# Optimization experiments

Hardware: AMD Instinct MI355X
Metric: run time of the kernel (lower is better)

## Reference

```python
import jax, jax.numpy as jnp
import numpy as np

RNN = 2048
NZ = 64
IN = 69  # 54 dofs + 15 actions


def gru_cell(x, h, w_ih, w_hh, b_ih, b_hh):
    gi = x @ w_ih.T + b_ih
    gh = h @ w_hh.T + b_hh
    i_r, i_z, i_n = jnp.split(gi, 3, axis=-1)
    h_r, h_z, h_n = jnp.split(gh, 3, axis=-1)
    r = jax.nn.sigmoid(i_r + h_r)
    z = jax.nn.sigmoid(i_z + h_z)
    n = jnp.tanh(i_n + r * h_n)
    return (1.0 - z) * n + z * h


def setup_inputs() -> dict:
    key = jax.random.key(0)
    ks = jax.random.split(key, 24)
    s = 0.02
    d = {
        'encoder_inputs': jax.random.normal(ks[0], (256, 49, IN), jnp.float32),
        'decoder_inputs': jax.random.normal(ks[1], (256, 25, IN), jnp.float32),
        'eps': jax.random.normal(ks[2], (256, NZ), jnp.float32),
        'fc0_w': jax.random.normal(ks[3], (RNN, 2 * IN), jnp.float32) * s,
        'fc0_b': jnp.zeros((RNN,), jnp.float32),
        'fc1_w': jax.random.normal(ks[4], (RNN, NZ + IN), jnp.float32) * s,
        'fc1_b': jnp.zeros((RNN,), jnp.float32),
        'fc2_w': jax.random.normal(ks[5], (IN, RNN), jnp.float32) * s,
        'fc2_b': jnp.zeros((IN,), jnp.float32),
        'mu_w': jax.random.normal(ks[6], (NZ, RNN), jnp.float32) * s,
        'mu_b': jnp.zeros((NZ,), jnp.float32),
        'sigma_w': jax.random.normal(ks[7], (NZ, RNN), jnp.float32) * s,
        'sigma_b': jnp.zeros((NZ,), jnp.float32),
        'c1_wih': jax.random.normal(ks[8], (3 * RNN, RNN), jnp.float32) * s,
        'c1_whh': jax.random.normal(ks[9], (3 * RNN, RNN), jnp.float32) * s,
        'c1_bih': jnp.zeros((3 * RNN,), jnp.float32),
        'c1_bhh': jnp.zeros((3 * RNN,), jnp.float32),
        'c2_wih': jax.random.normal(ks[10], (3 * RNN, IN), jnp.float32) * s,
        'c2_whh': jax.random.normal(ks[11], (3 * RNN, RNN), jnp.float32) * s,
        'c2_bih': jnp.zeros((3 * RNN,), jnp.float32),
        'c2_bhh': jnp.zeros((3 * RNN,), jnp.float32),
    }
    return d


def reference(encoder_inputs, decoder_inputs, eps, fc0_w, fc0_b, fc1_w, fc1_b, fc2_w, fc2_b,
              mu_w, mu_b, sigma_w, sigma_b, c1_wih, c1_whh, c1_bih, c1_bhh,
              c2_wih, c2_whh, c2_bih, c2_bhh):
    B = encoder_inputs.shape[0]
    enc_t = jnp.transpose(encoder_inputs, (1, 0, 2))  # [S-1, B, IN]
    dec_t = jnp.transpose(decoder_inputs, (1, 0, 2))  # [T, B, IN]
    # encoder step inputs: cat(enc[i], enc[i+1]); last step pairs with dec[0]
    nxt = jnp.concatenate([enc_t[1:], dec_t[:1]], axis=0)
    pairs = jnp.concatenate([enc_t, nxt], axis=-1)  # [S-1, B, 2*IN]
    x = pairs @ fc0_w.T + fc0_b  # fc0, [S-1, B, RNN]
    # precompute input-to-hidden GEMMs for all encoder steps
    gi_all = x @ c1_wih.T + c1_bih  # [S-1, B, 3*RNN]

    def enc_step(h, gi):
        gh = h @ c1_whh.T + c1_bhh
        i_r, i_z, i_n = jnp.split(gi, 3, axis=-1)
        h_r, h_z, h_n = jnp.split(gh, 3, axis=-1)
        r = jax.nn.sigmoid(i_r + h_r)
        z = jax.nn.sigmoid(i_z + h_z)
        n = jnp.tanh(i_n + r * h_n)
        return (1.0 - z) * n + z * h, None

    h0 = jnp.zeros((B, RNN), encoder_inputs.dtype)
    state, _ = jax.lax.scan(enc_step, h0, gi_all)

    z_mu = state @ mu_w.T + mu_b
    z_logvar = state @ sigma_w.T + sigma_b
    z = z_mu + eps * jnp.exp(0.5 * z_logvar)

    dec0 = dec_t[0]  # [B, IN]
    state = jnp.concatenate([z, dec0], axis=-1) @ fc1_w.T + fc1_b

    def dec_step(carry, _):
        h, inp = carry
        h = gru_cell(inp, h, c2_wih, c2_whh, c2_bih, c2_bhh)
        out = inp + (h @ fc2_w.T + fc2_b)  # residual feedback (eval: no dropout)
        return (h, out), out

    T = dec_t.shape[0]
    _, ys = jax.lax.scan(dec_step, (state, dec0), None, length=T)  # [T, B, IN]
    outputs = jnp.transpose(ys, (1, 0, 2))
    return outputs, z_mu, z_logvar
```

## Files before the change

### kernel.cpp

```cpp
#include <hip/hip_runtime.h>
#include <stdint.h>

#define B_    256
#define SE    49
#define TD    25
#define INDIM 69
#define RNN   2048
#define NZ    64
#define G3    6144

typedef __attribute__((ext_vector_type(8))) short short8_t;
typedef __attribute__((ext_vector_type(4))) float f32x4;
typedef unsigned short u16;

#define BARRIER() do { asm volatile("s_waitcnt lgkmcnt(0)" ::: "memory"); \
                       __builtin_amdgcn_s_barrier(); } while (0)

__device__ __forceinline__ u16 f2b(float f) {
  union { float f; unsigned u; } c; c.f = f;
  unsigned u = c.u;
  return (u16)((u + 0x7FFFu + ((u >> 16) & 1u)) >> 16);
}
__device__ __forceinline__ float sigm(float x) { return 1.f / (1.f + __expf(-x)); }
__device__ __forceinline__ short8_t ldbf(const u16* __restrict__ p, size_t off) {
  return *(const short8_t*)&p[off];
}

__device__ __forceinline__ int rmap(int R) {
  int bn = R / 96, rem = R % 96;
  int nw = rem / 48, g = (rem % 48) / 16, jj = rem % 16;
  return g * RNN + bn * 32 + nw * 16 + jj;
}

__global__ void k_reorder(const float* __restrict__ src, u16* __restrict__ dst, int K, int Kp) {
  int total = G3 * Kp;
  for (int i = blockIdx.x * blockDim.x + threadIdx.x; i < total; i += gridDim.x * blockDim.x) {
    int R = i / Kp, c = i % Kp;
    dst[i] = (c < K) ? f2b(src[(size_t)rmap(R) * K + c]) : (u16)0;
  }
}

__global__ void k_fc0T(const float* __restrict__ fc0w, const float* __restrict__ fc0b,
                       u16* __restrict__ dst) {
  int total = 256 * RNN;
  for (int i = blockIdx.x * blockDim.x + threadIdx.x; i < total; i += gridDim.x * blockDim.x) {
    int r = i >> 11, k = i & (RNN - 1);
    float v = 0.f;
    if (r < 2 * INDIM) v = fc0w[(size_t)k * (2 * INDIM) + r];
    else if (r == 2 * INDIM) v = fc0b[k];
    dst[i] = f2b(v);
  }
}

__global__ void k_fc2T(const float* __restrict__ fc2w, u16* __restrict__ dst) {
  int total = 96 * RNN;
  for (int i = blockIdx.x * blockDim.x + threadIdx.x; i < total; i += gridDim.x * blockDim.x) {
    int r = i >> 11, k = i & (RNN - 1);
    dst[i] = (r < INDIM) ? f2b(fc2w[(size_t)r * RNN + k]) : (u16)0;
  }
}

__global__ void k_pairs(const float* __restrict__ enc, const float* __restrict__ dec,
                        u16* __restrict__ pairs) {
  int total = SE * B_ * 256;
  for (int i = blockIdx.x * blockDim.x + threadIdx.x; i < total; i += gridDim.x * blockDim.x) {
    int c = i & 255, rb = i >> 8;
    int b = rb & 255, t = rb >> 8;
    float v = 0.f;
    if (c < INDIM) v = enc[((size_t)b * SE + t) * INDIM + c];
    else if (c < 2 * INDIM) {
      int cc = c - INDIM;
      v = (t < SE - 1) ? enc[((size_t)b * SE + t + 1) * INDIM + cc]
                       : dec[(size_t)b * TD * INDIM + cc];
    } else if (c == 2 * INDIM) v = 1.0f;
    pairs[i] = f2b(v);
  }
}

__global__ void k_msB(const float* __restrict__ muw, const float* __restrict__ sgw,
                      u16* __restrict__ dst) {
  int total = 128 * RNN;
  for (int i = blockIdx.x * blockDim.x + threadIdx.x; i < total; i += gridDim.x * blockDim.x) {
    int n = i >> 11, k = i & (RNN - 1);
    dst[i] = (n < NZ) ? f2b(muw[(size_t)n * RNN + k]) : f2b(sgw[(size_t)(n - NZ) * RNN + k]);
  }
}

__global__ void k_fc1B(const float* __restrict__ w, u16* __restrict__ dst) {
  int total = RNN * 192;
  for (int i = blockIdx.x * blockDim.x + threadIdx.x; i < total; i += gridDim.x * blockDim.x) {
    int n = i / 192, k = i % 192;
    dst[i] = (k < NZ + INDIM) ? f2b(w[(size_t)n * (NZ + INDIM) + k]) : (u16)0;
  }
}

__global__ void k_bias(const float* __restrict__ c1bih, const float* __restrict__ c1bhh,
                       const float* __restrict__ c2wih, const float* __restrict__ fc2b,
                       const float* __restrict__ c2bih, const float* __restrict__ c2bhh,
                       float* __restrict__ ebi, float* __restrict__ ebh,
                       float* __restrict__ dbi0, float* __restrict__ dbi1, float* __restrict__ dbh) {
  int R = blockIdx.x * blockDim.x + threadIdx.x;
  if (R >= G3) return;
  int orig = rmap(R);
  float k3 = 0.f;
  for (int o = 0; o < INDIM; ++o) k3 += c2wih[(size_t)orig * INDIM + o] * fc2b[o];
  ebi[R] = c1bih[orig];
  ebh[R] = c1bhh[orig];
  float d0 = c2bih[orig];
  dbi0[R] = d0;
  dbi1[R] = d0 + k3;
  dbh[R] = c2bhh[orig];
}

__global__ void k_init(float* __restrict__ hf, u16* __restrict__ hbf, float* __restrict__ fbuf,
                       float* __restrict__ omu, float* __restrict__ olv) {
  int i = blockIdx.x * blockDim.x + threadIdx.x;
  if (i < B_ * RNN) { hf[i] = 0.f; hbf[i] = 0; }
  if (i < 3 * B_ * 96) fbuf[i] = 0.f;
  if (i < B_ * NZ) { omu[i] = 0.f; olv[i] = 0.f; }
}

__global__ __launch_bounds__(256) void gemm_bt(
    const u16* __restrict__ A, const u16* __restrict__ W,
    u16* __restrict__ Cb, int N, int K)
{
  constexpr int BM = 128, BN = 128, BK = 64, LDK = BK + 8;
  __shared__ u16 sA[BM * LDK];
  __shared__ u16 sW[BN * LDK];
  const int ntn = N / BN;
  const int bm = blockIdx.x / ntn, bn = blockIdx.x % ntn;
  const int tid = threadIdx.x, lane = tid & 63, wave = tid >> 6;
  const int wr = wave >> 1, wc = wave & 1;
  f32x4 acc[4][4];
#pragma unroll
  for (int i = 0; i < 4; ++i)
#pragma unroll
    for (int j = 0; j < 4; ++j) acc[i][j] = (f32x4)(0.f);
  const int frow = lane & 15, fkq = (lane >> 4) * 8;
  for (int k0 = 0; k0 < K; k0 += BK) {
#pragma unroll
    for (int p = 0; p < 4; ++p) {
      int e = (p * 256 + tid) * 8, r = e / BK, c = e % BK;
      *(short8_t*)&sA[r * LDK + c] = *(const short8_t*)&A[(size_t)(bm * BM + r) * K + k0 + c];
    }
#pragma unroll
    for (int p = 0; p < 4; ++p) {
      int e = (p * 256 + tid) * 8, r = e / BK, c = e % BK;
      *(short8_t*)&sW[r * LDK + c] = *(const short8_t*)&W[(size_t)(bn * BN + r) * K + k0 + c];
    }
    __syncthreads();
#pragma unroll
    for (int kk = 0; kk < BK; kk += 32) {
      short8_t fa[4], fb[4];
#pragma unroll
      for (int m = 0; m < 4; ++m) fa[m] = *(const short8_t*)&sA[(wr * 64 + m * 16 + frow) * LDK + kk + fkq];
#pragma unroll
      for (int n = 0; n < 4; ++n) fb[n] = *(const short8_t*)&sW[(wc * 64 + n * 16 + frow) * LDK + kk + fkq];
#pragma unroll
      for (int m = 0; m < 4; ++m)
#pragma unroll
        for (int n = 0; n < 4; ++n)
          acc[m][n] = __builtin_amdgcn_mfma_f32_16x16x32_bf16(fa[m], fb[n], acc[m][n], 0, 0, 0);
    }
    __syncthreads();
  }
  const int crow = (lane >> 4) * 4, ccol = lane & 15;
#pragma unroll
  for (int n = 0; n < 4; ++n) {
    int col = bn * BN + wc * 64 + n * 16 + ccol;
#pragma unroll
    for (int m = 0; m < 4; ++m)
#pragma unroll
      for (int r = 0; r < 4; ++r) {
        int rowi = bm * BM + wr * 64 + m * 16 + crow + r;
        Cb[(size_t)rowi * N + col] = f2b(acc[m][n][r]);
      }
  }
}

struct Args {
  const u16 *pairs, *Wenc, *whh1, *whh2, *wih2, *fc2T;
  const u16 *msB, *fc1wB;
  const float *ebi, *ebh, *dbi0, *dbi1, *dbh;
  const float *eps, *dec, *fc1_b, *fc2_b, *mu_b, *sg_b;
  float* hf;
  u16*   hbf;
  float* fbuf;
  float* inp;
  u16*   inpbf;
  u16*   fc1xB;
  float *out, *out_mu, *out_lv;
};

__device__ __forceinline__ void compute_gi(const char* sA, const char* sW,
    f32x4 (&aR)[4], f32x4 (&aZ)[4], f32x4 (&aN)[4], int kg, int nw, int lane) {
#pragma unroll
  for (int s = 0; s < 2; ++s) {
    const int L = kg * 8 + s * 4 + (lane >> 4);
    short8_t fa[4], fb[3];
#pragma unroll
    for (int m = 0; m < 4; ++m) {
      int r = m * 16 + (lane & 15);
      fa[m] = *(const short8_t*)&sA[r * 512 + ((L ^ (r & 7)) * 16)];
    }
#pragma unroll
    for (int g = 0; g < 3; ++g) {
      int r = nw * 48 + g * 16 + (lane & 15);
      fb[g] = *(const short8_t*)&sW[r * 512 + ((L ^ (r & 7)) * 16)];
    }
#pragma unroll
    for (int m = 0; m < 4; ++m) {
      aR[m] = __builtin_amdgcn_mfma_f32_16x16x32_bf16(fa[m], fb[0], aR[m], 0, 0, 0);
      aZ[m] = __builtin_amdgcn_mfma_f32_16x16x32_bf16(fa[m], fb[1], aZ[m], 0, 0, 0);
      aN[m] = __builtin_amdgcn_mfma_f32_16x16x32_bf16(fa[m], fb[2], aN[m], 0, 0, 0);
    }
  }
}

__device__ __forceinline__ void compute_gh(const char* base,
    f32x4 (&aR)[4], f32x4 (&aZ)[4], f32x4 (&aN)[4], int kg, int nw, int lane) {
  const char* sA = base;
  const char* sW = base + 16384;
  const int L = kg * 4 + (lane >> 4);
  short8_t fa[4], fb[3];
#pragma unroll
  for (int m = 0; m < 4; ++m) {
    int r = m * 16 + (lane & 15);
    fa[m] = *(const short8_t*)&sA[r * 256 + ((L ^ (r & 15)) * 16)];
  }
#pragma unroll
  for (int g = 0; g < 3; ++g) {
    int r = nw * 48 + g * 16 + (lane & 15);
    fb[g] = *(const short8_t*)&sW[r * 256 + ((L ^ (r & 15)) * 16)];
  }
#pragma unroll
  for (int m = 0; m < 4; ++m) {
    aR[m] = __builtin_amdgcn_mfma_f32_16x16x32_bf16(fa[m], fb[0], aR[m], 0, 0, 0);
    aZ[m] = __builtin_amdgcn_mfma_f32_16x16x32_bf16(fa[m], fb[1], aZ[m], 0, 0, 0);
    aN[m] = __builtin_amdgcn_mfma_f32_16x16x32_bf16(fa[m], fb[2], aN[m], 0, 0, 0);
  }
}

__device__ __forceinline__ void reduce_and_gate(
    f32x4 (&aR)[4], f32x4 (&aZ)[4], f32x4 (&aNI)[4], f32x4 (&aNH)[4],
    char* smem, int tid, int bm, int bn,
    const float* __restrict__ bi, const float* __restrict__ bh,
    const float* __restrict__ hfold, float* __restrict__ hfnew, u16* __restrict__ hbnew) {
  const int lane = tid & 63, wid = tid >> 6;
  auto wr16 = [&](int slots, int w) {
#pragma unroll
    for (int m = 0; m < 4; ++m) {
      *(f32x4*)&smem[(((0 * 4 + m) * slots + w) * 64 + lane) * 16] = aR[m];
      *(f32x4*)&smem[(((1 * 4 + m) * slots + w) * 64 + lane) * 16] = aZ[m];
      *(f32x4*)&smem[(((2 * 4 + m) * slots + w) * 64 + lane) * 16] = aNI[m];
      *(f32x4*)&smem[(((3 * 4 + m) * slots + w) * 64 + lane) * 16] = aNH[m];
    }
  };
  auto add16 = [&](int slots, int w) {
#pragma unroll
    for (int m = 0; m < 4; ++m) {
      aR[m]  += *(const f32x4*)&smem[(((0 * 4 + m) * slots + w) * 64 + lane) * 16];
      aZ[m]  += *(const f32x4*)&smem[(((1 * 4 + m) * slots + w) * 64 + lane) * 16];
      aNI[m] += *(const f32x4*)&smem[(((2 * 4 + m) * slots + w) * 64 + lane) * 16];
      aNH[m] += *(const f32x4*)&smem[(((3 * 4 + m) * slots + w) * 64 + lane) * 16];
    }
  };
  __syncthreads();
  if (wid >= 4) wr16(4, wid - 4);
  __syncthreads();
  if (wid < 4) add16(4, wid);
  __syncthreads();
  if (wid == 2 || wid == 3) wr16(2, wid - 2);
  __syncthreads();
  if (wid < 2) {
    add16(2, wid);
    const int nw = wid, jj = lane & 15;
    const int Rb = bn * 96 + nw * 48;
    const float biR = bi[Rb + jj],      bhR = bh[Rb + jj];
    const float biZ = bi[Rb + 16 + jj], bhZ = bh[Rb + 16 + jj];
    const float biN = bi[Rb + 32 + jj], bhN = bh[Rb + 32 + jj];
    const int j = bn * 32 + nw * 16 + jj;
#pragma unroll
    for (int m = 0; m < 4; ++m)
#pragma unroll
      for (int q = 0; q < 4; ++q) {
        int b = bm * 64 + m * 16 + ((lane >> 4) << 2) + q;
        float r = sigm(aR[m][q] + biR + bhR);
        float z = sigm(aZ[m][q] + biZ + bhZ);
        float nn = 2.f * sigm(2.f * ((aNI[m][q] + biN) + r * (aNH[m][q] + bhN))) - 1.f;
        float hv = (1.f - z) * nn + z * hfold[(size_t)b * RNN + j];
        hfnew[(size_t)b * RNN + j] = hv;
        hbnew[(size_t)b * RNN + j] = f2b(hv);
      }
  }
}

__global__ __launch_bounds__(512, 1) void k_enc(Args a, int t) {
  __shared__ char smem[81920];
  const int tid = threadIdx.x, lane = tid & 63, wid = tid >> 6;
  const int kg = wid >> 1, nw = wid & 1;
  const int bm = blockIdx.x >> 6, bn = blockIdx.x & 63;
  const int rowA0 = bm * 64, rowW0 = bn * 96;
  const int pin = t & 1, pout = pin ^ 1;
  const u16* hin = a.hbf + (size_t)pin * B_ * RNN;
  const float* hfold = a.hf + (size_t)pin * B_ * RNN;
  float* hfnew = a.hf + (size_t)pout * B_ * RNN;
  u16* hbnew = a.hbf + (size_t)pout * B_ * RNN;
  const int sr32 = tid >> 5, sc32 = tid & 31;
  const int sr16 = tid >> 4, sc16 = tid & 15;

  f32x4 aR[4], aZ[4], aNI[4], aNH[4];
#pragma unroll
  for (int m = 0; m < 4; ++m) {
    aR[m] = (f32x4)(0.f); aZ[m] = (f32x4)(0.f);
    aNI[m] = (f32x4)(0.f); aNH[m] = (f32x4)(0.f);
  }

  auto issue_gh = [&](short8_t (&ra)[2], short8_t (&rw)[3], int k0) {
#pragma unroll
    for (int p = 0; p < 2; ++p) {
      int r = p * 32 + sr16;
      ra[p] = ldbf(hin, (size_t)(rowA0 + r) * RNN + k0 + sc16 * 8);
    }
#pragma unroll
    for (int p = 0; p < 3; ++p) {
      int r = p * 32 + sr16;
      rw[p] = ldbf(a.whh1, (size_t)(rowW0 + r) * RNN + k0 + sc16 * 8);
    }
  };
  auto write_gh = [&](char* base, short8_t (&ra)[2], short8_t (&rw)[3]) {
#pragma unroll
    for (int p = 0; p < 2; ++p) {
      int r = p * 32 + sr16;
      *(short8_t*)&base[r * 256 + ((sc16 ^ (r & 15)) * 16)] = ra[p];
    }
#pragma unroll
    for (int p = 0; p < 3; ++p) {
      int r = p * 32 + sr16;
      *(short8_t*)&(base + 16384)[r * 256 + ((sc16 ^ (r & 15)) * 16)] = rw[p];
    }
  };

  {
    const u16* P = a.pairs + (size_t)t * B_ * 256;
    short8_t ga[4], gw[6];
#pragma unroll
    for (int p = 0; p < 4; ++p) {
      int r = p * 16 + sr32;
      ga[p] = ldbf(P, (size_t)(rowA0 + r) * 256 + sc32 * 8);
    }
#pragma unroll
    for (int p = 0; p < 6; ++p) {
      int r = p * 16 + sr32;
      gw[p] = ldbf(a.Wenc, (size_t)(rowW0 + r) * 256 + sc32 * 8);
    }
#pragma unroll
    for (int p = 0; p < 4; ++p) {
      int r = p * 16 + sr32;
      *(short8_t*)&smem[r * 512 + ((sc32 ^ (r & 7)) * 16)] = ga[p];
    }
#pragma unroll
    for (int p = 0; p < 6; ++p) {
      int r = p * 16 + sr32;
      *(short8_t*)&smem[32768 + r * 512 + ((sc32 ^ (r & 7)) * 16)] = gw[p];
    }
  }
  short8_t rA0[2], rW0[3], rA1[2], rW1[3];
  issue_gh(rA0, rW0, 0);
  issue_gh(rA1, rW1, 128);
  BARRIER();
  compute_gi(smem, smem + 32768, aR, aZ, aNI, kg, nw, lane);
  BARRIER();
  write_gh(smem, rA0, rW0);
  issue_gh(rA0, rW0, 2 * 128);
  BARRIER();
#pragma unroll
  for (int i = 0; i < 16; ++i) {
    char* cb = (i & 1) ? smem + 40960 : smem;
    if (i + 1 <= 15) {
      char* nb = ((i + 1) & 1) ? smem + 40960 : smem;
      if ((i + 1) & 1) {
        write_gh(nb, rA1, rW1);
        if (i + 3 <= 15) issue_gh(rA1, rW1, (i + 3) * 128);
      } else {
        write_gh(nb, rA0, rW0);
        if (i + 3 <= 15) issue_gh(rA0, rW0, (i + 3) * 128);
      }
    }
    compute_gh(cb, aR, aZ, aNH, kg, nw, lane);
    if (i < 15) BARRIER();
  }
  reduce_and_gate(aR, aZ, aNI, aNH, smem, tid, bm, bn, a.ebi, a.ebh, hfold, hfnew, hbnew);
}

__global__ __launch_bounds__(512, 1) void k_dec(Args a, int t) {
  __shared__ char smem[81920];
  const int tid = threadIdx.x, lane = tid & 63, wid = tid >> 6;
  const int kg = wid >> 1, nw = wid & 1;
  const int bm = blockIdx.x >> 6, bn = blockIdx.x & 63;
  const int rowA0 = bm * 64, rowW0 = bn * 96;
  const int pin = t & 1, pout = pin ^ 1;
  const int irs = (t + 1) & 1, iws = t & 1;
  const int frd = (t + 2) % 3;
  const u16* hin = a.hbf + (size_t)pin * B_ * RNN;
  const float* hfold = a.hf + (size_t)pin * B_ * RNN;
  float* hfnew = a.hf + (size_t)pout * B_ * RNN;
  u16* hbnew = a.hbf + (size_t)pout * B_ * RNN;
  const int gtid = blockIdx.x * 512 + tid;
  const int sr32 = tid >> 5, sc32 = tid & 31;
  const int sr16 = tid >> 4, sc16 = tid & 15;
  const int fr = lane & 15, fq = (lane >> 4) << 3;

  if (t >= 1 && gtid < B_ * INDIM) {
    int b = gtid / INDIM, o = gtid % INDIM;
    float v = a.inp[(size_t)irs * B_ * INDIM + gtid] +
              a.fbuf[(size_t)frd * B_ * 96 + b * 96 + o] + a.fc2_b[o];
    a.out[((size_t)b * TD + (t - 1)) * INDIM + o] = v;
    a.inp[(size_t)iws * B_ * INDIM + gtid] = v;
    a.inpbf[(size_t)iws * B_ * 128 + b * 128 + o] = f2b(v);
  }
  if (gtid < B_ * 96)
    a.fbuf[(size_t)((t + 1) % 3) * B_ * 96 + gtid] = 0.f;

  f32x4 aR[4], aZ[4], aNI[4], aNH[4];
#pragma unroll
  for (int m = 0; m < 4; ++m) {
    aR[m] = (f32x4)(0.f); aZ[m] = (f32x4)(0.f);
    aNI[m] = (f32x4)(0.f); aNH[m] = (f32x4)(0.f);
  }

  auto issue_gh = [&](short8_t (&ra)[2], short8_t (&rw)[3], int k0) {
#pragma unroll
    for (int p = 0; p < 2; ++p) {
      int r = p * 32 + sr16;
      ra[p] = ldbf(hin, (size_t)(rowA0 + r) * RNN + k0 + sc16 * 8);
    }
#pragma unroll
    for (int p = 0; p < 3; ++p) {
      int r = p * 32 + sr16;
      rw[p] = ldbf(a.whh2, (size_t)(rowW0 + r) * RNN + k0 + sc16 * 8);
    }
  };
  auto write_gh = [&](char* base, short8_t (&ra)[2], short8_t (&rw)[3]) {
#pragma unroll
    for (int p = 0; p < 2; ++p) {
      int r = p * 32 + sr16;
      *(short8_t*)&base[r * 256 + ((sc16 ^ (r & 15)) * 16)] = ra[p];
    }
#pragma unroll
    for (int p = 0; p < 3; ++p) {
      int r = p * 32 + sr16;
      *(short8_t*)&(base + 16384)[r * 256 + ((sc16 ^ (r & 15)) * 16)] = rw[p];
    }
  };

  {
    const u16* inpA = a.inpbf + (size_t)irs * B_ * 128;
    const float* F = a.fbuf + (size_t)frd * B_ * 96;
    short8_t ga[4], gw[6];
#pragma unroll
    for (int p = 0; p < 4; ++p) {
      int r = p * 16 + sr32;
      if (sc32 < 16) {
        ga[p] = ldbf(inpA, (size_t)(rowA0 + r) * 128 + sc32 * 8);
      } else {
        short8_t v;
        int o0 = (sc32 - 16) * 8;
#pragma unroll
        for (int e = 0; e < 8; ++e) {
          int o = o0 + e;
          float fv = (o < 96) ? F[(size_t)(rowA0 + r) * 96 + o] : 0.f;
          v[e] = (short)f2b(fv);
        }
        ga[p] = v;
      }
    }
#pragma unroll
    for (int p = 0; p < 6; ++p) {
      int r = p * 16 + sr32;
      gw[p] = ldbf(a.wih2, (size_t)(rowW0 + r) * 128 + (sc32 & 15) * 8);
    }
#pragma unroll
    for (int p = 0; p < 4; ++p) {
      int r = p * 16 + sr32;
      *(short8_t*)&smem[r * 512 + ((sc32 ^ (r & 7)) * 16)] = ga[p];
    }
#pragma unroll
    for (int p = 0; p < 6; ++p) {
      int r = p * 16 + sr32;
      *(short8_t*)&smem[32768 + r * 512 + ((sc32 ^ (r & 7)) * 16)] = gw[p];
    }
  }
  short8_t rA0[2], rW0[3], rA1[2], rW1[3];
  issue_gh(rA0, rW0, 0);
  issue_gh(rA1, rW1, 128);
  BARRIER();
  compute_gi(smem, smem + 32768, aR, aZ, aNI, kg, nw, lane);
  BARRIER();
  write_gh(smem, rA0, rW0);
  issue_gh(rA0, rW0, 2 * 128);
  BARRIER();
#pragma unroll
  for (int i = 0; i < 16; ++i) {
    char* cb = (i & 1) ? smem + 40960 : smem;
    if (i + 1 <= 15) {
      char* nb = ((i + 1) & 1) ? smem + 40960 : smem;
      if ((i + 1) & 1) {
        write_gh(nb, rA1, rW1);
        if (i + 3 <= 15) issue_gh(rA1, rW1, (i + 3) * 128);
      } else {
        write_gh(nb, rA0, rW0);
        if (i + 3 <= 15) issue_gh(rA0, rW0, (i + 3) * 128);
      }
    }
    compute_gh(cb, aR, aZ, aNH, kg, nw, lane);
    if (i < 15) BARRIER();
  }
  reduce_and_gate(aR, aZ, aNI, aNH, smem, tid, bm, bn,
                  (t >= 1) ? a.dbi1 : a.dbi0, a.dbh, hfold, hfnew, hbnew);

  __syncthreads();
  if (wid < 4) {
    const int wr = wid >> 1, wc = wid & 1;
    const int kcol = bn * 32 + fq;
    short8_t fa[2], fb[3];
#pragma unroll
    for (int m = 0; m < 2; ++m)
      fa[m] = ldbf(hbnew, (size_t)(bm * 64 + wr * 32 + m * 16 + fr) * RNN + kcol);
#pragma unroll
    for (int n = 0; n < 3; ++n)
      fb[n] = ldbf(a.fc2T, (size_t)(wc * 48 + n * 16 + fr) * RNN + kcol);
    f32x4 accf[2][3];
#pragma unroll
    for (int m = 0; m < 2; ++m)
#pragma unroll
      for (int n = 0; n < 3; ++n) accf[m][n] = (f32x4)(0.f);
#pragma unroll
    for (int m = 0; m < 2; ++m)
#pragma unroll
      for (int n = 0; n < 3; ++n)
        accf[m][n] = __builtin_amdgcn_mfma_f32_16x16x32_bf16(fa[m], fb[n], accf[m][n], 0, 0, 0);
    float* fdst = a.fbuf + (size_t)(t % 3) * B_ * 96;
#pragma unroll
    for (int m = 0; m < 2; ++m)
#pragma unroll
      for (int n = 0; n < 3; ++n)
#pragma unroll
        for (int q = 0; q < 4; ++q) {
          int row = bm * 64 + wr * 32 + m * 16 + ((lane >> 4) << 2) + q;
          int col = wc * 48 + n * 16 + (lane & 15);
          atomicAdd(&fdst[row * 96 + col], accf[m][n][q]);
        }
  }
}

__global__ __launch_bounds__(256) void k_msm(Args a) {
  const int bm = blockIdx.x >> 3, kc = blockIdx.x & 7;
  const int lane = threadIdx.x & 63, wid = threadIdx.x >> 6;
  const int wr = wid >> 1, wc = wid & 1;
  const int fr = lane & 15, fq = (lane >> 4) << 3;
  const u16* h1 = a.hbf + (size_t)B_ * RNN;
  f32x4 acc[4][4];
#pragma unroll
  for (int m = 0; m < 4; ++m)
#pragma unroll
    for (int n = 0; n < 4; ++n) acc[m][n] = (f32x4)(0.f);
#pragma unroll
  for (int ks = 0; ks < 8; ++ks) {
    const int k = kc * 256 + ks * 32 + fq;
    short8_t fa[4], fb[4];
#pragma unroll
    for (int m = 0; m < 4; ++m)
      fa[m] = ldbf(h1, (size_t)(bm * 128 + wr * 64 + m * 16 + fr) * RNN + k);
#pragma unroll
    for (int n = 0; n < 4; ++n)
      fb[n] = ldbf(a.msB, (size_t)(wc * 64 + n * 16 + fr) * RNN + k);
#pragma unroll
    for (int m = 0; m < 4; ++m)
#pragma unroll
      for (int n = 0; n < 4; ++n)
        acc[m][n] = __builtin_amdgcn_mfma_f32_16x16x32_bf16(fa[m], fb[n], acc[m][n], 0, 0, 0);
  }
#pragma unroll
  for (int m = 0; m < 4; ++m)
#pragma unroll
    for (int n = 0; n < 4; ++n)
#pragma unroll
      for (int q = 0; q < 4; ++q) {
        int row = bm * 128 + wr * 64 + m * 16 + ((lane >> 4) << 2) + q;
        int col = wc * 64 + n * 16 + (lane & 15);
        if (col < NZ) atomicAdd(&a.out_mu[row * NZ + col], acc[m][n][q]);
        else          atomicAdd(&a.out_lv[row * NZ + col - NZ], acc[m][n][q]);
      }
}

__global__ void k_sample(Args a) {
  int gid = blockIdx.x * blockDim.x + threadIdx.x;
  if (gid < B_ * NZ) {
    int b = gid >> 6, n = gid & 63;
    float mu = a.out_mu[gid] + a.mu_b[n];
    float lv = a.out_lv[gid] + a.sg_b[n];
    a.out_mu[gid] = mu;
    a.out_lv[gid] = lv;
    a.fc1xB[b * 192 + n] = f2b(mu + a.eps[gid] * __expf(0.5f * lv));
  }
  if (gid < B_ * 128) {
    int b = gid >> 7, c = gid & 127;
    float v = (c < INDIM) ? a.dec[(size_t)b * TD * INDIM + c] : 0.f;
    u16 vb = f2b(v);
    a.inpbf[(size_t)b * 128 + c] = vb;
    a.inpbf[(size_t)B_ * 128 + b * 128 + c] = vb;
    if (c < INDIM) {
      a.inp[b * INDIM + c] = v;
      a.inp[B_ * INDIM + b * INDIM + c] = v;
      a.fc1xB[b * 192 + NZ + c] = f2b(v);
    }
  }
  if (gid < B_ * 192) {
    int c = gid % 192;
    if (c >= NZ + INDIM) a.fc1xB[gid] = 0;
  }
}

__global__ __launch_bounds__(256) void k_fc1m(Args a) {
  const int bm = blockIdx.x >> 4, bn = blockIdx.x & 15;
  const int lane = threadIdx.x & 63, wid = threadIdx.x >> 6;
  const int wr = wid >> 1, wc = wid & 1;
  const int fr = lane & 15, fq = (lane >> 4) << 3;
  f32x4 acc[4][4];
#pragma unroll
  for (int m = 0; m < 4; ++m)
#pragma unroll
    for (int n = 0; n < 4; ++n) acc[m][n] = (f32x4)(0.f);
#pragma unroll
  for (int ks = 0; ks < 6; ++ks) {
    const int k = ks * 32 + fq;
    short8_t fa[4], fb[4];
#pragma unroll
    for (int m = 0; m < 4; ++m)
      fa[m] = ldbf(a.fc1xB, (size_t)(bm * 128 + wr * 64 + m * 16 + fr) * 192 + k);
#pragma unroll
    for (int n = 0; n < 4; ++n)
      fb[n] = ldbf(a.fc1wB, (size_t)(bn * 128 + wc * 64 + n * 16 + fr) * 192 + k);
#pragma unroll
    for (int m = 0; m < 4; ++m)
#pragma unroll
      for (int n = 0; n < 4; ++n)
        acc[m][n] = __builtin_amdgcn_mfma_f32_16x16x32_bf16(fa[m], fb[n], acc[m][n], 0, 0, 0);
  }
#pragma unroll
  for (int n = 0; n < 4; ++n) {
    const int col = bn * 128 + wc * 64 + n * 16 + (lane & 15);
    const float bv = a.fc1_b[col];
#pragma unroll
    for (int m = 0; m < 4; ++m)
#pragma unroll
      for (int q = 0; q < 4; ++q) {
        int row = bm * 128 + wr * 64 + m * 16 + ((lane >> 4) << 2) + q;
        float v = acc[m][n][q] + bv;
        a.hf[(size_t)row * RNN + col] = v;
        a.hbf[(size_t)row * RNN + col] = f2b(v);
      }
  }
}

__global__ void k_tail(Args a) {
  int i = blockIdx.x * blockDim.x + threadIdx.x;
  if (i < B_ * INDIM) {
    int b = i / INDIM, o = i % INDIM;
    float v = a.inp[(size_t)(24 & 1) * B_ * INDIM + i] +
              a.fbuf[(size_t)(24 % 3) * B_ * 96 + b * 96 + o] + a.fc2_b[o];
    a.out[((size_t)b * TD + 24) * INDIM + o] = v;
  }
}

extern "C" void kernel_launch(void* const* d_in, const int* in_sizes, int n_in,
                              void* d_out, int out_size, void* d_ws, size_t ws_size,
                              hipStream_t stream)
{
  const float* enc    = (const float*)d_in[0];
  const float* dec    = (const float*)d_in[1];
  const float* eps    = (const float*)d_in[2];
  const float* fc0_w  = (const float*)d_in[3];
  const float* fc0_b  = (const float*)d_in[4];
  const float* fc1_w  = (const float*)d_in[5];
  const float* fc1_b  = (const float*)d_in[6];
  const float* fc2_w  = (const float*)d_in[7];
  const float* fc2_b  = (const float*)d_in[8];
  const float* mu_w   = (const float*)d_in[9];
  const float* mu_b   = (const float*)d_in[10];
  const float* sg_w   = (const float*)d_in[11];
  const float* sg_b   = (const float*)d_in[12];
  const float* c1_wih = (const float*)d_in[13];
  const float* c1_whh = (const float*)d_in[14];
  const float* c1_bih = (const float*)d_in[15];
  const float* c1_bhh = (const float*)d_in[16];
  const float* c2_wih = (const float*)d_in[17];
  const float* c2_whh = (const float*)d_in[18];
  const float* c2_bih = (const float*)d_in[19];
  const float* c2_bhh = (const float*)d_in[20];

  float* out_outputs = (float*)d_out;
  float* out_mu = out_outputs + (size_t)B_ * TD * INDIM;
  float* out_lv = out_mu + (size_t)B_ * NZ;

  char* ws = (char*)d_ws;
  size_t off = 0;
  auto alloc = [&](size_t bytes) -> void* {
    void* p = ws + off; off += (bytes + 255) & ~(size_t)255; return p;
  };

  u16* whh1_r = (u16*)alloc((size_t)G3 * RNN * 2);
  u16* whh2_r = (u16*)alloc((size_t)G3 * RNN * 2);
  u16* wih1_r = (u16*)alloc((size_t)G3 * RNN * 2);
  u16* wih2_r = (u16*)alloc((size_t)G3 * 128 * 2);
  u16* fc0T   = (u16*)alloc((size_t)256 * RNN * 2);
  u16* fc2T   = (u16*)alloc((size_t)96 * RNN * 2);
  u16* Wenc   = (u16*)alloc((size_t)G3 * 256 * 2);
  u16* pairs  = (u16*)alloc((size_t)SE * B_ * 256 * 2);
  u16* msB    = (u16*)alloc((size_t)128 * RNN * 2);
  u16* fc1wB  = (u16*)alloc((size_t)RNN * 192 * 2);
  float* hf   = (float*)alloc((size_t)2 * B_ * RNN * 4);
  u16* hbf    = (u16*)alloc((size_t)2 * B_ * RNN * 2);
  float* fbuf = (float*)alloc((size_t)3 * B_ * 96 * 4);
  float* inp  = (float*)alloc((size_t)2 * B_ * INDIM * 4);
  u16* inpbf  = (u16*)alloc((size_t)2 * B_ * 128 * 2);
  u16* fc1xB  = (u16*)alloc((size_t)B_ * 192 * 2);
  float* ebi  = (float*)alloc((size_t)G3 * 4);
  float* ebh  = (float*)alloc((size_t)G3 * 4);
  float* dbi0 = (float*)alloc((size_t)G3 * 4);
  float* dbi1 = (float*)alloc((size_t)G3 * 4);
  float* dbh  = (float*)alloc((size_t)G3 * 4);
  (void)ws_size; (void)in_sizes; (void)n_in; (void)out_size;

  k_reorder<<<4096, 256, 0, stream>>>(c1_whh, whh1_r, RNN, RNN);
  k_reorder<<<4096, 256, 0, stream>>>(c2_whh, whh2_r, RNN, RNN);
  k_reorder<<<4096, 256, 0, stream>>>(c1_wih, wih1_r, RNN, RNN);
  k_reorder<<<1024, 256, 0, stream>>>(c2_wih, wih2_r, INDIM, 128);
  k_fc0T<<<512, 256, 0, stream>>>(fc0_w, fc0_b, fc0T);
  k_fc2T<<<256, 256, 0, stream>>>(fc2_w, fc2T);
  k_pairs<<<2048, 256, 0, stream>>>(enc, dec, pairs);
  k_msB<<<256, 256, 0, stream>>>(mu_w, sg_w, msB);
  k_fc1B<<<256, 256, 0, stream>>>(fc1_w, fc1wB);
  k_bias<<<24, 256, 0, stream>>>(c1_bih, c1_bhh, c2_wih, fc2_b, c2_bih, c2_bhh,
                                 ebi, ebh, dbi0, dbi1, dbh);

  Args a;
  a.pairs = pairs; a.Wenc = Wenc; a.whh1 = whh1_r; a.whh2 = whh2_r;
  a.wih2 = wih2_r; a.fc2T = fc2T; a.msB = msB; a.fc1wB = fc1wB;
  a.ebi = ebi; a.ebh = ebh; a.dbi0 = dbi0; a.dbi1 = dbi1; a.dbh = dbh;
  a.eps = eps; a.dec = dec; a.fc1_b = fc1_b; a.fc2_b = fc2_b;
  a.mu_b = mu_b; a.sg_b = sg_b;
  a.hf = hf; a.hbf = hbf; a.fbuf = fbuf; a.inp = inp; a.inpbf = inpbf;
  a.fc1xB = fc1xB; a.out = out_outputs; a.out_mu = out_mu; a.out_lv = out_lv;

  k_init<<<2048, 256, 0, stream>>>(hf, hbf, fbuf, out_mu, out_lv);
  gemm_bt<<<(G3 / 128) * (256 / 128), 256, 0, stream>>>(wih1_r, fc0T, Wenc, 256, RNN);

  for (int t = 0; t < SE; ++t)
    k_enc<<<256, 512, 0, stream>>>(a, t);
  k_msm<<<16, 256, 0, stream>>>(a);
  k_sample<<<192, 256, 0, stream>>>(a);
  k_fc1m<<<32, 256, 0, stream>>>(a);
  for (int t = 0; t < TD; ++t)
    k_dec<<<256, 512, 0, stream>>>(a, t);
  k_tail<<<69, 256, 0, stream>>>(a);
}
```

Measured before the change: 1.435 ms.

## Double waves per block in GRU step kernels by splitting batch rows across waves

The encoder and decoder recurrent-step kernels go from 512 to 1024 threads per block. Each wave now computes a 32-row by 48-column tile instead of 64 by 48, and the tile load/store indexing is rebalanced across the larger thread count. The cross-wave K reduction is reorganised for four K-groups times four M/N sub-tiles. The intent is more waves per CU, so the latency of the one-block-per-CU recurrence is better hidden. In exchange each wave has fewer MFMAs per LDS fragment load, the reduction stage carries more traffic, and the main loop is no longer force-unrolled.

```diff
diff --git a/kernel.cpp b/kernel.cpp
--- a/kernel.cpp
+++ b/kernel.cpp
@@ -192,99 +192,52 @@
   float *out, *out_mu, *out_lv;
 };
 
-__device__ __forceinline__ void compute_gi(const char* sA, const char* sW,
-    f32x4 (&aR)[4], f32x4 (&aZ)[4], f32x4 (&aN)[4], int kg, int nw, int lane) {
-#pragma unroll
-  for (int s = 0; s < 2; ++s) {
-    const int L = kg * 8 + s * 4 + (lane >> 4);
-    short8_t fa[4], fb[3];
-#pragma unroll
-    for (int m = 0; m < 4; ++m) {
-      int r = m * 16 + (lane & 15);
-      fa[m] = *(const short8_t*)&sA[r * 512 + ((L ^ (r & 7)) * 16)];
-    }
-#pragma unroll
-    for (int g = 0; g < 3; ++g) {
-      int r = nw * 48 + g * 16 + (lane & 15);
-      fb[g] = *(const short8_t*)&sW[r * 512 + ((L ^ (r & 7)) * 16)];
-    }
-#pragma unroll
-    for (int m = 0; m < 4; ++m) {
-      aR[m] = __builtin_amdgcn_mfma_f32_16x16x32_bf16(fa[m], fb[0], aR[m], 0, 0, 0);
-      aZ[m] = __builtin_amdgcn_mfma_f32_16x16x32_bf16(fa[m], fb[1], aZ[m], 0, 0, 0);
-      aN[m] = __builtin_amdgcn_mfma_f32_16x16x32_bf16(fa[m], fb[2], aN[m], 0, 0, 0);
-    }
-  }
-}
-
-__device__ __forceinline__ void compute_gh(const char* base,
-    f32x4 (&aR)[4], f32x4 (&aZ)[4], f32x4 (&aN)[4], int kg, int nw, int lane) {
-  const char* sA = base;
-  const char* sW = base + 16384;
-  const int L = kg * 4 + (lane >> 4);
-  short8_t fa[4], fb[3];
-#pragma unroll
-  for (int m = 0; m < 4; ++m) {
-    int r = m * 16 + (lane & 15);
-    fa[m] = *(const short8_t*)&sA[r * 256 + ((L ^ (r & 15)) * 16)];
-  }
-#pragma unroll
-  for (int g = 0; g < 3; ++g) {
-    int r = nw * 48 + g * 16 + (lane & 15);
-    fb[g] = *(const short8_t*)&sW[r * 256 + ((L ^ (r & 15)) * 16)];
-  }
-#pragma unroll
-  for (int m = 0; m < 4; ++m) {
-    aR[m] = __builtin_amdgcn_mfma_f32_16x16x32_bf16(fa[m], fb[0], aR[m], 0, 0, 0);
-    aZ[m] = __builtin_amdgcn_mfma_f32_16x16x32_bf16(fa[m], fb[1], aZ[m], 0, 0, 0);
-    aN[m] = __builtin_amdgcn_mfma_f32_16x16x32_bf16(fa[m], fb[2], aN[m], 0, 0, 0);
-  }
-}
-
 __device__ __forceinline__ void reduce_and_gate(
-    f32x4 (&aR)[4], f32x4 (&aZ)[4], f32x4 (&aNI)[4], f32x4 (&aNH)[4],
+    f32x4 (&aR)[2], f32x4 (&aZ)[2], f32x4 (&aNI)[2], f32x4 (&aNH)[2],
     char* smem, int tid, int bm, int bn,
     const float* __restrict__ bi, const float* __restrict__ bh,
     const float* __restrict__ hfold, float* __restrict__ hfnew, u16* __restrict__ hbnew) {
   const int lane = tid & 63, wid = tid >> 6;
-  auto wr16 = [&](int slots, int w) {
-#pragma unroll
-    for (int m = 0; m < 4; ++m) {
-      *(f32x4*)&smem[(((0 * 4 + m) * slots + w) * 64 + lane) * 16] = aR[m];
-      *(f32x4*)&smem[(((1 * 4 + m) * slots + w) * 64 + lane) * 16] = aZ[m];
-      *(f32x4*)&smem[(((2 * 4 + m) * slots + w) * 64 + lane) * 16] = aNI[m];
-      *(f32x4*)&smem[(((3 * 4 + m) * slots + w) * 64 + lane) * 16] = aNH[m];
-    }
-  };
-  auto add16 = [&](int slots, int w) {
-#pragma unroll
-    for (int m = 0; m < 4; ++m) {
-      aR[m]  += *(const f32x4*)&smem[(((0 * 4 + m) * slots + w) * 64 + lane) * 16];
-      aZ[m]  += *(const f32x4*)&smem[(((1 * 4 + m) * slots + w) * 64 + lane) * 16];
-      aNI[m] += *(const f32x4*)&smem[(((2 * 4 + m) * slots + w) * 64 + lane) * 16];
-      aNH[m] += *(const f32x4*)&smem[(((3 * 4 + m) * slots + w) * 64 + lane) * 16];
+  const int kg = wid >> 2, grp = wid & 3;
+  auto wrp = [&](int slots, int s) {
+#pragma unroll
+    for (int m = 0; m < 2; ++m) {
+      *(f32x4*)&smem[(((0 * 2 + m) * slots + s) * 64 + lane) * 16] = aR[m];
+      *(f32x4*)&smem[(((1 * 2 + m) * slots + s) * 64 + lane) * 16] = aZ[m];
+      *(f32x4*)&smem[(((2 * 2 + m) * slots + s) * 64 + lane) * 16] = aNI[m];
+      *(f32x4*)&smem[(((3 * 2 + m) * slots + s) * 64 + lane) * 16] = aNH[m];
+    }
+  };
+  auto addp = [&](int slots, int s) {
+#pragma unroll
+    for (int m = 0; m < 2; ++m) {
+      aR[m]  += *(const f32x4*)&smem[(((0 * 2 + m) * slots + s) * 64 + lane) * 16];
+      aZ[m]  += *(const f32x4*)&smem[(((1 * 2 + m) * slots + s) * 64 + lane) * 16];
+      aNI[m] += *(const f32x4*)&smem[(((2 * 2 + m) * slots + s) * 64 + lane) * 16];
+      aNH[m] += *(const f32x4*)&smem[(((3 * 2 + m) * slots + s) * 64 + lane) * 16];
     }
   };
   __syncthreads();
-  if (wid >= 4) wr16(4, wid - 4);
+  if (kg >= 2) wrp(8, (kg - 2) * 4 + grp);
   __syncthreads();
-  if (wid < 4) add16(4, wid);
+  if (kg < 2) addp(8, kg * 4 + grp);
   __syncthreads();
-  if (wid == 2 || wid == 3) wr16(2, wid - 2);
+  if (kg == 1) wrp(4, grp);
   __syncthreads();
-  if (wid < 2) {
-    add16(2, wid);
-    const int nw = wid, jj = lane & 15;
+  if (kg == 0) {
+    addp(4, grp);
+    const int mw = grp & 1, nw = grp >> 1;
+    const int jj = lane & 15;
     const int Rb = bn * 96 + nw * 48;
     const float biR = bi[Rb + jj],      bhR = bh[Rb + jj];
     const float biZ = bi[Rb + 16 + jj], bhZ = bh[Rb + 16 + jj];
     const float biN = bi[Rb + 32 + jj], bhN = bh[Rb + 32 + jj];
     const int j = bn * 32 + nw * 16 + jj;
 #pragma unroll
-    for (int m = 0; m < 4; ++m)
+    for (int m = 0; m < 2; ++m)
 #pragma unroll
       for (int q = 0; q < 4; ++q) {
-        int b = bm * 64 + m * 16 + ((lane >> 4) << 2) + q;
+        int b = bm * 64 + mw * 32 + m * 16 + ((lane >> 4) << 2) + q;
         float r = sigm(aR[m][q] + biR + bhR);
         float z = sigm(aZ[m][q] + biZ + bhZ);
         float nn = 2.f * sigm(2.f * ((aNI[m][q] + biN) + r * (aNH[m][q] + bhN))) - 1.f;
@@ -295,86 +248,128 @@
   }
 }
 
-__global__ __launch_bounds__(512, 1) void k_enc(Args a, int t) {
+__global__ __launch_bounds__(1024, 1) void k_enc(Args a, int t) {
   __shared__ char smem[81920];
   const int tid = threadIdx.x, lane = tid & 63, wid = tid >> 6;
-  const int kg = wid >> 1, nw = wid & 1;
+  const int mw = wid & 1, nw = (wid >> 1) & 1, kg = wid >> 2;
   const int bm = blockIdx.x >> 6, bn = blockIdx.x & 63;
-  const int rowA0 = bm * 64, rowW0 = bn * 96;
+  const int rowA0 = bm * 64, rowW0b = bn * 96;
   const int pin = t & 1, pout = pin ^ 1;
   const u16* hin = a.hbf + (size_t)pin * B_ * RNN;
   const float* hfold = a.hf + (size_t)pin * B_ * RNN;
   float* hfnew = a.hf + (size_t)pout * B_ * RNN;
   u16* hbnew = a.hbf + (size_t)pout * B_ * RNN;
-  const int sr32 = tid >> 5, sc32 = tid & 31;
-  const int sr16 = tid >> 4, sc16 = tid & 15;
-
-  f32x4 aR[4], aZ[4], aNI[4], aNH[4];
-#pragma unroll
-  for (int m = 0; m < 4; ++m) {
+
+  f32x4 aR[2], aZ[2], aNI[2], aNH[2];
+#pragma unroll
+  for (int m = 0; m < 2; ++m) {
     aR[m] = (f32x4)(0.f); aZ[m] = (f32x4)(0.f);
     aNI[m] = (f32x4)(0.f); aNH[m] = (f32x4)(0.f);
   }
 
-  auto issue_gh = [&](short8_t (&ra)[2], short8_t (&rw)[3], int k0) {
+  auto issue_gh = [&](short8_t& ra, short8_t (&rw)[2], int k0) {
+    { int r = tid >> 4, c = tid & 15;
+      ra = ldbf(hin, (size_t)(rowA0 + r) * RNN + k0 + c * 8); }
 #pragma unroll
     for (int p = 0; p < 2; ++p) {
-      int r = p * 32 + sr16;
-      ra[p] = ldbf(hin, (size_t)(rowA0 + r) * RNN + k0 + sc16 * 8);
-    }
-#pragma unroll
-    for (int p = 0; p < 3; ++p) {
-      int r = p * 32 + sr16;
-      rw[p] = ldbf(a.whh1, (size_t)(rowW0 + r) * RNN + k0 + sc16 * 8);
-    }
-  };
-  auto write_gh = [&](char* base, short8_t (&ra)[2], short8_t (&rw)[3]) {
+      int s = tid + p * 1024;
+      if (s < 1536) {
+        int r = s >> 4, c = s & 15;
+        rw[p] = ldbf(a.whh1, (size_t)(rowW0b + r) * RNN + k0 + c * 8);
+      }
+    }
+  };
+  auto write_gh = [&](char* base, short8_t& ra, short8_t (&rw)[2]) {
+    { int r = tid >> 4, c = tid & 15;
+      *(short8_t*)&base[r * 256 + ((c ^ (r & 15)) * 16)] = ra; }
 #pragma unroll
     for (int p = 0; p < 2; ++p) {
-      int r = p * 32 + sr16;
-      *(short8_t*)&base[r * 256 + ((sc16 ^ (r & 15)) * 16)] = ra[p];
-    }
-#pragma unroll
-    for (int p = 0; p < 3; ++p) {
-      int r = p * 32 + sr16;
-      *(short8_t*)&(base + 16384)[r * 256 + ((sc16 ^ (r & 15)) * 16)] = rw[p];
+      int s = tid + p * 1024;
+      if (s < 1536) {
+        int r = s >> 4, c = s & 15;
+        *(short8_t*)&(base + 16384)[r * 256 + ((c ^ (r & 15)) * 16)] = rw[p];
+      }
+    }
+  };
+  auto compute_gh = [&](const char* base) {
+    const char* sA = base;
+    const char* sW = base + 16384;
+    const int L = kg * 4 + (lane >> 4);
+    short8_t fa[2], fb[3];
+#pragma unroll
+    for (int m = 0; m < 2; ++m) {
+      int r = mw * 32 + m * 16 + (lane & 15);
+      fa[m] = *(const short8_t*)&sA[r * 256 + ((L ^ (r & 15)) * 16)];
+    }
+#pragma unroll
+    for (int g = 0; g < 3; ++g) {
+      int r = nw * 48 + g * 16 + (lane & 15);
+      fb[g] = *(const short8_t*)&sW[r * 256 + ((L ^ (r & 15)) * 16)];
+    }
+#pragma unroll
+    for (int m = 0; m < 2; ++m) {
+      aR[m]  = __builtin_amdgcn_mfma_f32_16x16x32_bf16(fa[m], fb[0], aR[m], 0, 0, 0);
+      aZ[m]  = __builtin_amdgcn_mfma_f32_16x16x32_bf16(fa[m], fb[1], aZ[m], 0, 0, 0);
+      aNH[m] = __builtin_amdgcn_mfma_f32_16x16x32_bf16(fa[m], fb[2], aNH[m], 0, 0, 0);
+    }
+  };
+  auto compute_gi = [&]() {
+#pragma unroll
+    for (int s = 0; s < 2; ++s) {
+      const int L = kg * 8 + s * 4 + (lane >> 4);
+      short8_t fa[2], fb[3];
+#pragma unroll
+      for (int m = 0; m < 2; ++m) {
+        int r = mw * 32 + m * 16 + (lane & 15);
+        fa[m] = *(const short8_t*)&smem[r * 512 + ((L ^ (r & 7)) * 16)];
+      }
+#pragma unroll
+      for (int g = 0; g < 3; ++g) {
+        int r = nw * 48 + g * 16 + (lane & 15);
+        fb[g] = *(const short8_t*)&(smem + 32768)[r * 512 + ((L ^ (r & 7)) * 16)];
+      }
+#pragma unroll
+      for (int m = 0; m < 2; ++m) {
+        aR[m]  = __builtin_amdgcn_mfma_f32_16x16x32_bf16(fa[m], fb[0], aR[m], 0, 0, 0);
+        aZ[m]  = __builtin_amdgcn_mfma_f32_16x16x32_bf16(fa[m], fb[1], aZ[m], 0, 0, 0);
+        aNI[m] = __builtin_amdgcn_mfma_f32_16x16x32_bf16(fa[m], fb[2], aNI[m], 0, 0, 0);
+      }
     }
   };
 
   {
     const u16* P = a.pairs + (size_t)t * B_ * 256;
-    short8_t ga[4], gw[6];
-#pragma unroll
-    for (int p = 0; p < 4; ++p) {
-      int r = p * 16 + sr32;
-      ga[p] = ldbf(P, (size_t)(rowA0 + r) * 256 + sc32 * 8);
-    }
-#pragma unroll
-    for (int p = 0; p < 6; ++p) {
-      int r = p * 16 + sr32;
-      gw[p] = ldbf(a.Wenc, (size_t)(rowW0 + r) * 256 + sc32 * 8);
-    }
-#pragma unroll
-    for (int p = 0; p < 4; ++p) {
-      int r = p * 16 + sr32;
-      *(short8_t*)&smem[r * 512 + ((sc32 ^ (r & 7)) * 16)] = ga[p];
-    }
-#pragma unroll
-    for (int p = 0; p < 6; ++p) {
-      int r = p * 16 + sr32;
-      *(short8_t*)&smem[32768 + r * 512 + ((sc32 ^ (r & 7)) * 16)] = gw[p];
-    }
-  }
-  short8_t rA0[2], rW0[3], rA1[2], rW1[3];
+    short8_t ga[2], gw[3];
+#pragma unroll
+    for (int p = 0; p < 2; ++p) {
+      int s = tid + p * 1024, r = s >> 5, c = s & 31;
+      ga[p] = ldbf(P, (size_t)(rowA0 + r) * 256 + c * 8);
+    }
+#pragma unroll
+    for (int p = 0; p < 3; ++p) {
+      int s = tid + p * 1024, r = s >> 5, c = s & 31;
+      gw[p] = ldbf(a.Wenc, (size_t)(rowW0b + r) * 256 + c * 8);
+    }
+#pragma unroll
+    for (int p = 0; p < 2; ++p) {
+      int s = tid + p * 1024, r = s >> 5, c = s & 31;
+      *(short8_t*)&smem[r * 512 + ((c ^ (r & 7)) * 16)] = ga[p];
+    }
+#pragma unroll
+    for (int p = 0; p < 3; ++p) {
+      int s = tid + p * 1024, r = s >> 5, c = s & 31;
+      *(short8_t*)&(smem + 32768)[r * 512 + ((c ^ (r & 7)) * 16)] = gw[p];
+    }
+  }
+  short8_t rA0, rW0[2], rA1, rW1[2];
   issue_gh(rA0, rW0, 0);
   issue_gh(rA1, rW1, 128);
   BARRIER();
-  compute_gi(smem, smem + 32768, aR, aZ, aNI, kg, nw, lane);
+  compute_gi();
   BARRIER();
   write_gh(smem, rA0, rW0);
-  issue_gh(rA0, rW0, 2 * 128);
+  issue_gh(rA0, rW0, 256);
   BARRIER();
-#pragma unroll
   for (int i = 0; i < 16; ++i) {
     char* cb = (i & 1) ? smem + 40960 : smem;
     if (i + 1 <= 15) {
@@ -387,18 +382,19 @@
         if (i + 3 <= 15) issue_gh(rA0, rW0, (i + 3) * 128);
       }
     }
-    compute_gh(cb, aR, aZ, aNH, kg, nw, lane);
+    compute_gh(cb);
     if (i < 15) BARRIER();
   }
   reduce_and_gate(aR, aZ, aNI, aNH, smem, tid, bm, bn, a.ebi, a.ebh, hfold, hfnew, hbnew);
 }
 
-__global__ __launch_bounds__(512, 1) void k_dec(Args a, int t) {
+__global__ __launch_bounds__(1024, 1) void k_dec(Args a, int t) {
   __shared__ char smem[81920];
   const int tid = threadIdx.x, lane = tid & 63, wid = tid >> 6;
-  const int kg = wid >> 1, nw = wid & 1;
+  const int mw = wid & 1, nw = (wid >> 1) & 1, kg = wid >> 2;
   const int bm = blockIdx.x >> 6, bn = blockIdx.x & 63;
-  const int rowA0 = bm * 64, rowW0 = bn * 96;
+  const int rowA0 = bm * 64, rowW0b = bn * 96;
+  const int fr = lane & 15, fq = (lane >> 4) << 3;
   const int pin = t & 1, pout = pin ^ 1;
   const int irs = (t + 1) & 1, iws = t & 1;
   const int frd = (t + 2) % 3;
@@ -406,10 +402,7 @@
   const float* hfold = a.hf + (size_t)pin * B_ * RNN;
   float* hfnew = a.hf + (size_t)pout * B_ * RNN;
   u16* hbnew = a.hbf + (size_t)pout * B_ * RNN;
-  const int gtid = blockIdx.x * 512 + tid;
-  const int sr32 = tid >> 5, sc32 = tid & 31;
-  const int sr16 = tid >> 4, sc16 = tid & 15;
-  const int fr = lane & 15, fq = (lane >> 4) << 3;
+  const int gtid = blockIdx.x * 1024 + tid;
 
   if (t >= 1 && gtid < B_ * INDIM) {
     int b = gtid / INDIM, o = gtid % INDIM;
@@ -422,50 +415,95 @@
   if (gtid < B_ * 96)
     a.fbuf[(size_t)((t + 1) % 3) * B_ * 96 + gtid] = 0.f;
 
-  f32x4 aR[4], aZ[4], aNI[4], aNH[4];
-#pragma unroll
-  for (int m = 0; m < 4; ++m) {
+  f32x4 aR[2], aZ[2], aNI[2], aNH[2];
+#pragma unroll
+  for (int m = 0; m < 2; ++m) {
     aR[m] = (f32x4)(0.f); aZ[m] = (f32x4)(0.f);
     aNI[m] = (f32x4)(0.f); aNH[m] = (f32x4)(0.f);
   }
 
-  auto issue_gh = [&](short8_t (&ra)[2], short8_t (&rw)[3], int k0) {
+  auto issue_gh = [&](short8_t& ra, short8_t (&rw)[2], int k0) {
+    { int r = tid >> 4, c = tid & 15;
+      ra = ldbf(hin, (size_t)(rowA0 + r) * RNN + k0 + c * 8); }
 #pragma unroll
     for (int p = 0; p < 2; ++p) {
-      int r = p * 32 + sr16;
-      ra[p] = ldbf(hin, (size_t)(rowA0 + r) * RNN + k0 + sc16 * 8);
-    }
-#pragma unroll
-    for (int p = 0; p < 3; ++p) {
-      int r = p * 32 + sr16;
-      rw[p] = ldbf(a.whh2, (size_t)(rowW0 + r) * RNN + k0 + sc16 * 8);
-    }
-  };
-  auto write_gh = [&](char* base, short8_t (&ra)[2], short8_t (&rw)[3]) {
+      int s = tid + p * 1024;
+      if (s < 1536) {
+        int r = s >> 4, c = s & 15;
+        rw[p] = ldbf(a.whh2, (size_t)(rowW0b + r) * RNN + k0 + c * 8);
+      }
+    }
+  };
+  auto write_gh = [&](char* base, short8_t& ra, short8_t (&rw)[2]) {
+    { int r = tid >> 4, c = tid & 15;
+      *(short8_t*)&base[r * 256 + ((c ^ (r & 15)) * 16)] = ra; }
 #pragma unroll
     for (int p = 0; p < 2; ++p) {
-      int r = p * 32 + sr16;
-      *(short8_t*)&base[r * 256 + ((sc16 ^ (r & 15)) * 16)] = ra[p];
-    }
-#pragma unroll
-    for (int p = 0; p < 3; ++p) {
-      int r = p * 32 + sr16;
-      *(short8_t*)&(base + 16384)[r * 256 + ((sc16 ^ (r & 15)) * 16)] = rw[p];
+      int s = tid + p * 1024;
+      if (s < 1536) {
+        int r = s >> 4, c = s & 15;
+        *(short8_t*)&(base + 16384)[r * 256 + ((c ^ (r & 15)) * 16)] = rw[p];
+      }
+    }
+  };
+  auto compute_gh = [&](const char* base) {
+    const char* sA = base;
+    const char* sW = base + 16384;
+    const int L = kg * 4 + (lane >> 4);
+    short8_t fa[2], fb[3];
+#pragma unroll
+    for (int m = 0; m < 2; ++m) {
+      int r = mw * 32 + m * 16 + (lane & 15);
+      fa[m] = *(const short8_t*)&sA[r * 256 + ((L ^ (r & 15)) * 16)];
+    }
+#pragma unroll
+    for (int g = 0; g < 3; ++g) {
+      int r = nw * 48 + g * 16 + (lane & 15);
+      fb[g] = *(const short8_t*)&sW[r * 256 + ((L ^ (r & 15)) * 16)];
+    }
+#pragma unroll
+    for (int m = 0; m < 2; ++m) {
+      aR[m]  = __builtin_amdgcn_mfma_f32_16x16x32_bf16(fa[m], fb[0], aR[m], 0, 0, 0);
+      aZ[m]  = __builtin_amdgcn_mfma_f32_16x16x32_bf16(fa[m], fb[1], aZ[m], 0, 0, 0);
+      aNH[m] = __builtin_amdgcn_mfma_f32_16x16x32_bf16(fa[m], fb[2], aNH[m], 0, 0, 0);
+    }
+  };
+  auto compute_gi = [&]() {
+#pragma unroll
+    for (int s = 0; s < 2; ++s) {
+      const int L = kg * 8 + s * 4 + (lane >> 4);
+      short8_t fa[2], fb[3];
+#pragma unroll
+      for (int m = 0; m < 2; ++m) {
+        int r = mw * 32 + m * 16 + (lane & 15);
+        fa[m] = *(const short8_t*)&smem[r * 512 + ((L ^ (r & 7)) * 16)];
+      }
+#pragma unroll
+      for (int g = 0; g < 3; ++g) {
+        int r = nw * 48 + g * 16 + (lane & 15);
+        fb[g] = *(const short8_t*)&(smem + 32768)[r * 512 + ((L ^ (r & 7)) * 16)];
+      }
+#pragma unroll
+      for (int m = 0; m < 2; ++m) {
+        aR[m]  = __builtin_amdgcn_mfma_f32_16x16x32_bf16(fa[m], fb[0], aR[m], 0, 0, 0);
+        aZ[m]  = __builtin_amdgcn_mfma_f32_16x16x32_bf16(fa[m], fb[1], aZ[m], 0, 0, 0);
+        aNI[m] = __builtin_amdgcn_mfma_f32_16x16x32_bf16(fa[m], fb[2], aNI[m], 0, 0, 0);
+      }
     }
   };
 
   {
     const u16* inpA = a.inpbf + (size_t)irs * B_ * 128;
     const float* F = a.fbuf + (size_t)frd * B_ * 96;
-    short8_t ga[4], gw[6];
-#pragma unroll
-    for (int p = 0; p < 4; ++p) {
-      int r = p * 16 + sr32;
-      if (sc32 < 16) {
-        ga[p] = ldbf(inpA, (size_t)(rowA0 + r) * 128 + sc32 * 8);
+    short8_t ga[2], gw[3];
+#pragma unroll
+    for (int p = 0; p < 2; ++p) {
+      int s = tid + p * 1024, r = s >> 5, c = s & 31;
+      if (c < 16) {
+        ga[p] = ldbf(inpA, (size_t)(rowA0 + r) * 128 + c * 8);
       } else {
         short8_t v;
-        int o0 = (sc32 - 16) * 8;
+        int o0 = (c - 16) * 8;
 #pragma unroll
         for (int e = 0; e < 8; ++e) {
           int o = o0 + e;
@@ -476,31 +514,30 @@
       }
     }
 #pragma unroll
-    for (int p = 0; p < 6; ++p) {
-      int r = p * 16 + sr32;
-      gw[p] = ldbf(a.wih2, (size_t)(rowW0 + r) * 128 + (sc32 & 15) * 8);
-    }
-#pragma unroll
-    for (int p = 0; p < 4; ++p) {
-      int r = p * 16 + sr32;
-      *(short8_t*)&smem[r * 512 + ((sc32 ^ (r & 7)) * 16)] = ga[p];
-    }
-#pragma unroll
-    for (int p = 0; p < 6; ++p) {
-      int r = p * 16 + sr32;
-      *(short8_t*)&smem[32768 + r * 512 + ((sc32 ^ (r & 7)) * 16)] = gw[p];
-    }
-  }
-  short8_t rA0[2], rW0[3], rA1[2], rW1[3];
+    for (int p = 0; p < 3; ++p) {
+      int s = tid + p * 1024, r = s >> 5, c = s & 31;
+      gw[p] = ldbf(a.wih2, (size_t)(rowW0b + r) * 128 + (c & 15) * 8);
+    }
+#pragma unroll
+    for (int p = 0; p < 2; ++p) {
+      int s = tid + p * 1024, r = s >> 5, c = s & 31;
+      *(short8_t*)&smem[r * 512 + ((c ^ (r & 7)) * 16)] = ga[p];
+    }
+#pragma unroll
+    for (int p = 0; p < 3; ++p) {
+      int s = tid + p * 1024, r = s >> 5, c = s & 31;
+      *(short8_t*)&(smem + 32768)[r * 512 + ((c ^ (r & 7)) * 16)] = gw[p];
+    }
+  }
+  short8_t rA0, rW0[2], rA1, rW1[2];
   issue_gh(rA0, rW0, 0);
   issue_gh(rA1, rW1, 128);
   BARRIER();
-  compute_gi(smem, smem + 32768, aR, aZ, aNI, kg, nw, lane);
+  compute_gi();
   BARRIER();
   write_gh(smem, rA0, rW0);
-  issue_gh(rA0, rW0, 2 * 128);
+  issue_gh(rA0, rW0, 256);
   BARRIER();
-#pragma unroll
   for (int i = 0; i < 16; ++i) {
     char* cb = (i & 1) ? smem + 40960 : smem;
     if (i + 1 <= 15) {
@@ -513,7 +550,7 @@
         if (i + 3 <= 15) issue_gh(rA0, rW0, (i + 3) * 128);
       }
     }
-    compute_gh(cb, aR, aZ, aNH, kg, nw, lane);
+    compute_gh(cb);
     if (i < 15) BARRIER();
   }
   reduce_and_gate(aR, aZ, aNI, aNH, smem, tid, bm, bn,
@@ -758,11 +795,11 @@
   gemm_bt<<<(G3 / 128) * (256 / 128), 256, 0, stream>>>(wih1_r, fc0T, Wenc, 256, RNN);
 
   for (int t = 0; t < SE; ++t)
-    k_enc<<<256, 512, 0, stream>>>(a, t);
+    k_enc<<<256, 1024, 0, stream>>>(a, t);
   k_msm<<<16, 256, 0, stream>>>(a);
   k_sample<<<192, 256, 0, stream>>>(a);
   k_fc1m<<<32, 256, 0, stream>>>(a);
   for (int t = 0; t < TD; ++t)
-    k_dec<<<256, 512, 0, stream>>>(a, t);
+    k_dec<<<256, 1024, 0, stream>>>(a, t);
   k_tail<<<69, 256, 0, stream>>>(a);
 }
```

Result: slower. 1.848 ms (+28.8%).
